# Performance work log

Hardware: AMD Instinct MI355X
Metric: run time of the kernel (lower is better)

Reference implementation:

```python
import jax, jax.numpy as jnp
import numpy as np

# Model dims (match init_kwargs)
B, H, W, C = 16, 6, 4096, 128
OVERLAP, NUM_PVQS, NUM_RVQS = 4, 3, 6
CB_DIM, CB_SIZE = 8, 1024
FIX = H * C                          # fix_dim = in_freq*in_dim = 768
HIDDEN = FIX * OVERLAP // NUM_PVQS   # 1024 per product group


def setup_inputs() -> dict:
    key = jax.random.key(0)
    k1, k2, k3, k4 = jax.random.split(key, 4)
    return {
        "z_e": jax.random.normal(k1, (B, H * W, C), jnp.float32),
        # per-(product-group, residual-stage) codebooks
        "embeds": jax.random.normal(k2, (NUM_PVQS, NUM_RVQS, CB_SIZE, CB_DIM), jnp.float32),
        # nn.Linear(hidden, codebook_dim, bias=False) stored as (hidden, cb_dim) so y = x @ W
        "proj_down": jax.random.normal(k3, (NUM_PVQS, HIDDEN, CB_DIM), jnp.float32) * (HIDDEN ** -0.5),
        "proj_up": jax.random.normal(k4, (NUM_PVQS, CB_DIM, HIDDEN), jnp.float32) * (CB_DIM ** -0.5),
        "num_streams": 6,
    }


def _l2n(x, eps=1e-12):
    return x / jnp.maximum(jnp.linalg.norm(x, axis=-1, keepdims=True), eps)


def _codebook(residual, embed):
    """One VQ codebook (l2norm variant): cdist + argmin + lookup + ST estimator.
    residual: (B, T, d); embed: (K, d)."""
    z = _l2n(residual)
    e = _l2n(embed)
    # squared euclidean distances (B, T, K)
    d = (z * z).sum(-1, keepdims=True) - 2.0 * jnp.einsum('btd,kd->btk', z, e) + (e * e).sum(-1)
    code = jnp.argmin(d, axis=-1)                      # (B, T) int
    q = jnp.take(e, code, axis=0)                      # (B, T, d)
    cb_loss = jnp.mean((q - jax.lax.stop_gradient(residual)) ** 2)
    cm_loss = jnp.mean((residual - jax.lax.stop_gradient(q)) ** 2)
    z_q = residual + jax.lax.stop_gradient(q - residual)   # straight-through
    return z_q, code, cb_loss, cm_loss


def reference(z_e, embeds, proj_down, proj_up, num_streams):
    # pre_process (dims=3): 'b (h w) c -> b w (c h)' then fold overlap frames
    x = z_e.reshape(B, H, W, C).transpose(0, 2, 3, 1).reshape(B, W, FIX)
    T = W // OVERLAP
    x = x.reshape(B, T, OVERLAP * FIX)

    zq_parts, code_parts = [], []
    cb_loss = 0.0
    cm_loss = 0.0
    for m in range(NUM_PVQS):
        xm = x[..., m * HIDDEN:(m + 1) * HIDDEN]
        residual = xm @ proj_down[m]                   # (B, T, CB_DIM)
        zq_m = jnp.zeros_like(residual)
        codes_m = []
        for i in range(num_streams):                   # residual VQ stages
            qi, ci, cb, cm = _codebook(residual, embeds[m, i])
            residual = residual - qi
            zq_m = zq_m + qi
            codes_m.append(ci)
            cb_loss = cb_loss + cb
            cm_loss = cm_loss + cm
        zq_parts.append(zq_m @ proj_up[m])             # (B, T, HIDDEN)
        code_parts.append(jnp.stack(codes_m, axis=1))  # (B, num_streams, T)

    zq = jnp.concatenate(zq_parts, axis=-1)            # (B, T, OVERLAP*FIX)
    codes = jnp.stack(code_parts, axis=2)              # (B, num_streams, num_pvqs, T)

    # post_process (dims=3): unfold overlap, 'b w (c h) -> b (h w) c'
    zq = zq.reshape(B, W, FIX).reshape(B, W, C, H).transpose(0, 3, 1, 2).reshape(B, H * W, C)
    return zq, codes, cb_loss / NUM_PVQS, cm_loss / NUM_PVQS
```

## Files before the change

kernel.cpp:

```cpp
#include <hip/hip_runtime.h>

#define BB        16
#define HH        6
#define WW        4096
#define CC        128
#define TT        1024
#define NTOK      16384
#define FIX       768
#define HID       1024
#define CBK       1024
#define CBD       8
#define NPVQ      3
#define NRVQ      6
#define ZQ_SIZE   50331648ull

#define OFF_ACC   0ull
#define OFF_EN64  16ull
#define OFF_EN32  (OFF_EN64 + 1179648ull)
#define OFF_PUT   (OFF_EN32 + 589824ull)
#define OFF_R     (OFF_PUT + 98304ull)
#define OFF_ZQ    (OFF_R + 3145728ull)

typedef float v2f __attribute__((ext_vector_type(2)));

__device__ __forceinline__ float dot32(const float* __restrict__ row,
                                       const v2f rn2[4]) {
    const float4* p4 = (const float4*)row;
    float4 e0 = p4[0], e1 = p4[1];
    v2f acc = {0.0f, 0.0f};
    v2f p;
    p.x = e0.x; p.y = e0.y; acc = __builtin_elementwise_fma(rn2[0], p, acc);
    p.x = e0.z; p.y = e0.w; acc = __builtin_elementwise_fma(rn2[1], p, acc);
    p.x = e1.x; p.y = e1.y; acc = __builtin_elementwise_fma(rn2[2], p, acc);
    p.x = e1.z; p.y = e1.w; acc = __builtin_elementwise_fma(rn2[3], p, acc);
    return acc.x + acc.y;
}

__global__ __launch_bounds__(256) void knorm(const float* __restrict__ emb,
                                             double* __restrict__ en64,
                                             float* __restrict__ en32) {
    int gid = blockIdx.x * 256 + threadIdx.x;
    if (gid >= NPVQ * NRVQ * CBK) return;
    const float* e = emb + (size_t)gid * CBD;
    double v[CBD];
    double s = 0.0;
#pragma unroll
    for (int d = 0; d < CBD; ++d) { v[d] = (double)e[d]; s += v[d] * v[d]; }
    double n = fmax(sqrt(s), 1e-12);
#pragma unroll
    for (int d = 0; d < CBD; ++d) {
        double q = v[d] / n;
        en64[(size_t)gid * CBD + d] = q;
        en32[(size_t)gid * CBD + d] = (float)q;
    }
}

__global__ __launch_bounds__(256) void kputr(const float* __restrict__ pu,
                                             float* __restrict__ pu_t) {
    int gid = blockIdx.x * 256 + threadIdx.x;
    if (gid >= NPVQ * CBD * HID) return;
    int j = gid & (HID - 1), md = gid >> 10;
    int m = md >> 3, d = md & 7;
    pu_t[((size_t)m * HID + j) * CBD + d] = pu[gid];
}

__global__ __launch_bounds__(384) void kproj(const float* __restrict__ ze,
                                             const float* __restrict__ pd,
                                             double* __restrict__ r_ws) {
    __shared__ float x[2][NPVQ * HID];
    const int tok0 = blockIdx.x * 2;
    const int b = tok0 >> 10, t0 = tok0 & 1023;
    const int tid = threadIdx.x;
    const size_t zbase = (size_t)b * (HH * WW * CC);
#pragma unroll
    for (int q = 0; q < 4; ++q) {
        int g = tid + 384 * q;
        int tk = g >= 768;
        int gg = g - tk * 768;
        int h = gg >> 7, v = gg & 127;
        const float4 val = *(const float4*)(ze + zbase + (size_t)(h * WW + (t0 + tk) * 4) * CC + v * 4);
        float vv[4] = {val.x, val.y, val.z, val.w};
#pragma unroll
        for (int e = 0; e < 4; ++e) {
            int oc = v * 4 + e, o = oc >> 7, c = oc & 127;
            x[tk][o * FIX + c * HH + h] = vv[e];
        }
    }
    __syncthreads();
    const int w = tid >> 6, l = tid & 63;
    const int tk = w >= 3, m = w - tk * 3;
    double acc[CBD] = {0, 0, 0, 0, 0, 0, 0, 0};
    for (int q = 0; q < 16; ++q) {
        int j = l + 64 * q;
        double xv = (double)x[tk][m * HID + j];
        const float* pr = pd + (size_t)(m * HID + j) * CBD;
#pragma unroll
        for (int d = 0; d < CBD; ++d) acc[d] = fma(xv, (double)pr[d], acc[d]);
    }
#pragma unroll
    for (int off = 32; off >= 1; off >>= 1) {
#pragma unroll
        for (int d = 0; d < CBD; ++d) acc[d] += __shfl_down(acc[d], off, 64);
    }
    if (l == 0) {
        double* rp = r_ws + ((size_t)m * NTOK + tok0 + tk) * CBD;
#pragma unroll
        for (int d = 0; d < CBD; ++d) rp[d] = acc[d];
    }
}

#define KV_WAVES    8
#define KV_THREADS  (KV_WAVES * 64)
#define KV_WSLICE   (CBK / KV_WAVES)
#define KV_EPS      2e-6f
#define KV_EPS_CAND 2e-6f

__global__ __launch_bounds__(KV_THREADS) void kvq(const double* __restrict__ en_all,
                                                  const float* __restrict__ es_all,
                                                  const double* __restrict__ r_ws,
                                                  float* __restrict__ zq_ws,
                                                  float* __restrict__ out,
                                                  const int* __restrict__ nsp,
                                                  double* __restrict__ accum) {
    __shared__ __align__(16) float tbl[CBK * CBD];
    __shared__ float  mb1[KV_THREADS];
    __shared__ float  mb2[KV_THREADS];
    __shared__ int    mbk[KV_THREADS];
    __shared__ double md64[KV_THREADS];
    __shared__ int    mk64[KV_THREADS];

    const int blk = blockIdx.x;
    const int m = blk >> 8, g = blk & 255;
    const int tid = threadIdx.x;
    const int w = tid >> 6, l = tid & 63;
    const int tok = g * 64 + l;
    const int b = tok >> 10, t = tok & 1023;
    const int ns = *nsp;

    double r[CBD];
    {
        const double* rp = r_ws + ((size_t)m * NTOK + tok) * CBD;
#pragma unroll
        for (int d = 0; d < CBD; ++d) r[d] = rp[d];
    }
    double zq[CBD] = {0, 0, 0, 0, 0, 0, 0, 0};
    double loss = 0.0;

    const int kl0 = w * KV_WSLICE;
    for (int i = 0; i < ns; ++i) {
        const double* en = en_all + ((size_t)(m * NRVQ + i)) * CBK * CBD;
        const float*  es = es_all + ((size_t)(m * NRVQ + i)) * CBK * CBD;
        double s = 0.0;
#pragma unroll
        for (int d = 0; d < CBD; ++d) s += r[d] * r[d];
        double inv = 1.0 / fmax(sqrt(s), 1e-12);
        v2f rn2[4];
#pragma unroll
        for (int d = 0; d < CBD; d += 2) {
            rn2[d >> 1].x = (float)(r[d] * inv);
            rn2[d >> 1].y = (float)(r[d + 1] * inv);
        }

        __syncthreads();
        {
            const float4* src = (const float4*)es;
            float4* dst = (float4*)tbl;
#pragma unroll
            for (int q = 0; q < 4; ++q) dst[tid + KV_THREADS * q] = src[tid + KV_THREADS * q];
        }
        __syncthreads();

        float b1 = -1e30f, b2 = -1e30f;
        int bk = kl0;
        for (int k = kl0; k < kl0 + KV_WSLICE; k += 4) {
            float dots[4];
#pragma unroll
            for (int u = 0; u < 4; ++u)
                dots[u] = dot32(tbl + (size_t)(k + u) * CBD, rn2);
#pragma unroll
            for (int u = 0; u < 4; ++u) {
                float dv = dots[u];
                if (dv > b1) { b2 = b1; b1 = dv; bk = k + u; }
                else if (dv > b2) { b2 = dv; }
            }
        }
        mb1[tid] = b1; mb2[tid] = b2; mbk[tid] = bk;
        __syncthreads();
        float B1 = mb1[l], B2 = mb2[l];
        int K = mbk[l];
#pragma unroll
        for (int w2 = 1; w2 < KV_WAVES; ++w2) {
            float c1 = mb1[w2 * 64 + l];
            float c2 = mb2[w2 * 64 + l];
            int   ck = mbk[w2 * 64 + l];
            if (c1 > B1) { B2 = fmaxf(B1, c2); B1 = c1; K = ck; }
            else         { B2 = fmaxf(B2, c1); }
        }
        int bbk = K;
        bool uncert = (B1 - B2) <= KV_EPS;
        if (__any(uncert)) {
            __syncthreads();
            double rb = -1e300;
            int rk = CBK;
            for (int k = kl0; k < kl0 + KV_WSLICE; ++k) {
                float dv = dot32(tbl + (size_t)k * CBD, rn2);
                if (uncert && dv >= B1 - KV_EPS_CAND) {
                    const double* e64 = en + (size_t)k * CBD;
                    double q0 = 0.0, q1 = 0.0;
#pragma unroll
                    for (int d = 0; d < CBD; d += 2) {
                        q0 = fma(r[d], e64[d], q0);
                        q1 = fma(r[d + 1], e64[d + 1], q1);
                    }
                    double dot = q0 + q1;
                    if (dot > rb || (dot == rb && k < rk)) { rb = dot; rk = k; }
                }
            }
            md64[tid] = rb; mk64[tid] = rk;
            __syncthreads();
            if (uncert) {
                double R = md64[l];
                int RK = mk64[l];
#pragma unroll
                for (int w2 = 1; w2 < KV_WAVES; ++w2) {
                    double d2 = md64[w2 * 64 + l];
                    int    k2 = mk64[w2 * 64 + l];
                    if (d2 > R || (d2 == R && k2 < RK)) { R = d2; RK = k2; }
                }
                bbk = RK;
            }
        }
        const double* qv = en + (size_t)bbk * CBD;
        if (w == 0) {
            double ls = 0.0;
#pragma unroll
            for (int d = 0; d < CBD; ++d) { double df = qv[d] - r[d]; ls += df * df; }
            loss += ls;
            out[ZQ_SIZE + ((size_t)(b * ns + i) * NPVQ + m) * TT + t] = (float)bbk;
        }
#pragma unroll
        for (int d = 0; d < CBD; ++d) { double q = qv[d]; r[d] -= q; zq[d] += q; }
    }

    if (w == 0) {
        float* zp = zq_ws + ((size_t)m * NTOK + tok) * CBD;
#pragma unroll
        for (int d = 0; d < CBD; ++d) zp[d] = (float)zq[d];
#pragma unroll
        for (int off = 32; off >= 1; off >>= 1) loss += __shfl_down(loss, off, 64);
        if (l == 0) atomicAdd(accum, loss);
    }
}

__global__ __launch_bounds__(256) void kout(const float* __restrict__ pu_t,
                                            const float* __restrict__ zq_ws,
                                            float* __restrict__ out,
                                            const int* __restrict__ nsp,
                                            const double* __restrict__ accum) {
    __shared__ float zl[32][NPVQ][CBD];
    const int blk = blockIdx.x;
    const int tok0 = blk * 32;
    const int b = tok0 >> 10, t0 = tok0 & 1023;
    const int tid = threadIdx.x;
#pragma unroll
    for (int q = 0; q < 3; ++q) {
        int ii = tid + 256 * q;
        int mm = ii >> 8, rem = ii & 255, tt = rem >> 3, d = rem & 7;
        zl[tt][mm][d] = zq_ws[((size_t)mm * NTOK + tok0 + tt) * CBD + d];
    }
    __syncthreads();
    const size_t obase = (size_t)b * (HH * WW * CC);
#pragma unroll 2
    for (int q = 0; q < 12; ++q) {
        int idx = tid + 256 * q;
        int h = idx >> 9, rem = idx & 511, o = rem >> 7, c = rem & 127;
        int f = o * FIX + c * HH + h;
        int m = f >> 10, j = f & 1023;
        const float4* p4 = (const float4*)(pu_t + ((size_t)m * HID + j) * CBD);
        float4 pa = p4[0], pb = p4[1];
        float pu8[CBD] = {pa.x, pa.y, pa.z, pa.w, pb.x, pb.y, pb.z, pb.w};
        size_t rowbase = obase + ((size_t)h * WW + t0 * 4 + o) * CC + c;
        for (int tt = 0; tt < 32; ++tt) {
            float y = 0.0f;
#pragma unroll
            for (int d = 0; d < CBD; ++d) y = fmaf(zl[tt][m][d], pu8[d], y);
            out[rowbase + (size_t)tt * 4 * CC] = y;
        }
    }
    if (blk == 0 && tid == 0) {
        int ns = *nsp;
        double s = *accum;
        float lv = (float)(s / (double)(NTOK * CBD * NPVQ));
        size_t lbase = ZQ_SIZE + (size_t)BB * ns * NPVQ * TT;
        out[lbase] = lv;
        out[lbase + 1] = lv;
    }
}

extern "C" void kernel_launch(void* const* d_in, const int* in_sizes, int n_in,
                              void* d_out, int out_size, void* d_ws, size_t ws_size,
                              hipStream_t stream) {
    const float* ze  = (const float*)d_in[0];
    const float* emb = (const float*)d_in[1];
    const float* pd  = (const float*)d_in[2];
    const float* pu  = (const float*)d_in[3];
    const int*   nsp = (const int*)d_in[4];
    float* out = (float*)d_out;
    char* ws = (char*)d_ws;

    double* accum = (double*)(ws + OFF_ACC);
    double* en64  = (double*)(ws + OFF_EN64);
    float*  en32  = (float*)(ws + OFF_EN32);
    float*  pu_t  = (float*)(ws + OFF_PUT);
    double* r_ws  = (double*)(ws + OFF_R);
    float*  zq_ws = (float*)(ws + OFF_ZQ);

    hipMemsetAsync(accum, 0, 16, stream);
    knorm<<<(NPVQ * NRVQ * CBK + 255) / 256, 256, 0, stream>>>(emb, en64, en32);
    kputr<<<(NPVQ * CBD * HID + 255) / 256, 256, 0, stream>>>(pu, pu_t);
    kproj<<<NTOK / 2, 384, 0, stream>>>(ze, pd, r_ws);
    kvq<<<NPVQ * (NTOK / 64), KV_THREADS, 0, stream>>>(en64, en32, r_ws, zq_ws, out, nsp, accum);
    kout<<<NTOK / 32, 256, 0, stream>>>(pu_t, zq_ws, out, nsp, accum);
}
```

Before: 330.0 us.

## Process four tokens per thread in VQ kernel to reuse LDS codebook loads

Each thread in the VQ search kernel now handles four tokens instead of one. Every codebook row read from LDS is reused across four token dot products, and the grid shrinks fourfold, so the per-block codebook staging into LDS is amortised over more tokens. zq accumulation moves from double to float. The costs are higher register pressure, managed with launch_bounds(512,2), fewer blocks (192) to fill the GPU, and extra syncthreads in the fallback path.

```diff
diff --git a/kernel.cpp b/kernel.cpp
--- a/kernel.cpp
+++ b/kernel.cpp
@@ -23,10 +23,8 @@
 
 typedef float v2f __attribute__((ext_vector_type(2)));
 
-__device__ __forceinline__ float dot32(const float* __restrict__ row,
-                                       const v2f rn2[4]) {
-    const float4* p4 = (const float4*)row;
-    float4 e0 = p4[0], e1 = p4[1];
+__device__ __forceinline__ float dot32v(const float4 e0, const float4 e1,
+                                        const v2f rn2[4]) {
     v2f acc = {0.0f, 0.0f};
     v2f p;
     p.x = e0.x; p.y = e0.y; acc = __builtin_elementwise_fma(rn2[0], p, acc);
@@ -111,54 +109,63 @@
 
 #define KV_WAVES    8
 #define KV_THREADS  (KV_WAVES * 64)
+#define KV_T        4
+#define KV_TPB      (64 * KV_T)
 #define KV_WSLICE   (CBK / KV_WAVES)
 #define KV_EPS      2e-6f
 #define KV_EPS_CAND 2e-6f
 
-__global__ __launch_bounds__(KV_THREADS) void kvq(const double* __restrict__ en_all,
-                                                  const float* __restrict__ es_all,
-                                                  const double* __restrict__ r_ws,
-                                                  float* __restrict__ zq_ws,
-                                                  float* __restrict__ out,
-                                                  const int* __restrict__ nsp,
-                                                  double* __restrict__ accum) {
+__global__ __launch_bounds__(KV_THREADS, 2) void kvq(const double* __restrict__ en_all,
+                                                     const float* __restrict__ es_all,
+                                                     const double* __restrict__ r_ws,
+                                                     float* __restrict__ zq_ws,
+                                                     float* __restrict__ out,
+                                                     const int* __restrict__ nsp,
+                                                     double* __restrict__ accum) {
     __shared__ __align__(16) float tbl[CBK * CBD];
-    __shared__ float  mb1[KV_THREADS];
-    __shared__ float  mb2[KV_THREADS];
-    __shared__ int    mbk[KV_THREADS];
+    __shared__ float  mb1[KV_T][KV_THREADS];
+    __shared__ float  mb2[KV_T][KV_THREADS];
+    __shared__ int    mbk[KV_T][KV_THREADS];
     __shared__ double md64[KV_THREADS];
     __shared__ int    mk64[KV_THREADS];
 
     const int blk = blockIdx.x;
-    const int m = blk >> 8, g = blk & 255;
+    const int m = blk / 64, gg = blk % 64;
     const int tid = threadIdx.x;
     const int w = tid >> 6, l = tid & 63;
-    const int tok = g * 64 + l;
-    const int b = tok >> 10, t = tok & 1023;
     const int ns = *nsp;
 
-    double r[CBD];
-    {
+    double r[KV_T][CBD];
+#pragma unroll
+    for (int j = 0; j < KV_T; ++j) {
+        const int tok = gg * KV_TPB + j * 64 + l;
         const double* rp = r_ws + ((size_t)m * NTOK + tok) * CBD;
 #pragma unroll
-        for (int d = 0; d < CBD; ++d) r[d] = rp[d];
-    }
-    double zq[CBD] = {0, 0, 0, 0, 0, 0, 0, 0};
+        for (int d = 0; d < CBD; ++d) r[j][d] = rp[d];
+    }
+    float zq[KV_T][CBD];
+#pragma unroll
+    for (int j = 0; j < KV_T; ++j)
+#pragma unroll
+        for (int d = 0; d < CBD; ++d) zq[j][d] = 0.0f;
     double loss = 0.0;
 
     const int kl0 = w * KV_WSLICE;
     for (int i = 0; i < ns; ++i) {
         const double* en = en_all + ((size_t)(m * NRVQ + i)) * CBK * CBD;
         const float*  es = es_all + ((size_t)(m * NRVQ + i)) * CBK * CBD;
-        double s = 0.0;
-#pragma unroll
-        for (int d = 0; d < CBD; ++d) s += r[d] * r[d];
-        double inv = 1.0 / fmax(sqrt(s), 1e-12);
-        v2f rn2[4];
-#pragma unroll
-        for (int d = 0; d < CBD; d += 2) {
-            rn2[d >> 1].x = (float)(r[d] * inv);
-            rn2[d >> 1].y = (float)(r[d + 1] * inv);
+        v2f rn2[KV_T][4];
+#pragma unroll
+        for (int j = 0; j < KV_T; ++j) {
+            double s = 0.0;
+#pragma unroll
+            for (int d = 0; d < CBD; ++d) s += r[j][d] * r[j][d];
+            double inv = 1.0 / fmax(sqrt(s), 1e-12);
+#pragma unroll
+            for (int d = 0; d < CBD; d += 2) {
+                rn2[j][d >> 1].x = (float)(r[j][d] * inv);
+                rn2[j][d >> 1].y = (float)(r[j][d + 1] * inv);
+            }
         }
 
         __syncthreads();
@@ -170,82 +177,119 @@
         }
         __syncthreads();
 
-        float b1 = -1e30f, b2 = -1e30f;
-        int bk = kl0;
-        for (int k = kl0; k < kl0 + KV_WSLICE; k += 4) {
-            float dots[4];
-#pragma unroll
-            for (int u = 0; u < 4; ++u)
-                dots[u] = dot32(tbl + (size_t)(k + u) * CBD, rn2);
-#pragma unroll
-            for (int u = 0; u < 4; ++u) {
-                float dv = dots[u];
-                if (dv > b1) { b2 = b1; b1 = dv; bk = k + u; }
-                else if (dv > b2) { b2 = dv; }
-            }
-        }
-        mb1[tid] = b1; mb2[tid] = b2; mbk[tid] = bk;
+        float b1[KV_T], b2[KV_T];
+        int bk[KV_T];
+#pragma unroll
+        for (int j = 0; j < KV_T; ++j) { b1[j] = -1e30f; b2[j] = -1e30f; bk[j] = kl0; }
+        for (int k = kl0; k < kl0 + KV_WSLICE; k += 2) {
+            const float4* pA = (const float4*)(tbl + (size_t)k * CBD);
+            float4 a0 = pA[0], a1 = pA[1];
+            float4 c0 = pA[2], c1 = pA[3];
+#pragma unroll
+            for (int j = 0; j < KV_T; ++j) {
+                float dA = dot32v(a0, a1, rn2[j]);
+                float dB = dot32v(c0, c1, rn2[j]);
+                if (dA > b1[j]) { b2[j] = b1[j]; b1[j] = dA; bk[j] = k; }
+                else if (dA > b2[j]) { b2[j] = dA; }
+                if (dB > b1[j]) { b2[j] = b1[j]; b1[j] = dB; bk[j] = k + 1; }
+                else if (dB > b2[j]) { b2[j] = dB; }
+            }
+        }
+#pragma unroll
+        for (int j = 0; j < KV_T; ++j) {
+            mb1[j][tid] = b1[j]; mb2[j][tid] = b2[j]; mbk[j][tid] = bk[j];
+        }
         __syncthreads();
-        float B1 = mb1[l], B2 = mb2[l];
-        int K = mbk[l];
-#pragma unroll
-        for (int w2 = 1; w2 < KV_WAVES; ++w2) {
-            float c1 = mb1[w2 * 64 + l];
-            float c2 = mb2[w2 * 64 + l];
-            int   ck = mbk[w2 * 64 + l];
-            if (c1 > B1) { B2 = fmaxf(B1, c2); B1 = c1; K = ck; }
-            else         { B2 = fmaxf(B2, c1); }
-        }
-        int bbk = K;
-        bool uncert = (B1 - B2) <= KV_EPS;
-        if (__any(uncert)) {
-            __syncthreads();
-            double rb = -1e300;
-            int rk = CBK;
+        float B1[KV_T], B2[KV_T];
+        int bbk[KV_T];
+        bool unc[KV_T];
+        bool anyu = false;
+#pragma unroll
+        for (int j = 0; j < KV_T; ++j) {
+            float x1 = mb1[j][l], x2 = mb2[j][l];
+            int xk = mbk[j][l];
+#pragma unroll
+            for (int w2 = 1; w2 < KV_WAVES; ++w2) {
+                float c1 = mb1[j][w2 * 64 + l];
+                float c2 = mb2[j][w2 * 64 + l];
+                int   ck = mbk[j][w2 * 64 + l];
+                if (c1 > x1) { x2 = fmaxf(x1, c2); x1 = c1; xk = ck; }
+                else         { x2 = fmaxf(x2, c1); }
+            }
+            B1[j] = x1; B2[j] = x2; bbk[j] = xk;
+            unc[j] = (x1 - x2) <= KV_EPS;
+            anyu |= unc[j];
+        }
+        if (__any(anyu)) {
+            double rb[KV_T];
+            int rk[KV_T];
+#pragma unroll
+            for (int j = 0; j < KV_T; ++j) { rb[j] = -1e300; rk[j] = CBK; }
             for (int k = kl0; k < kl0 + KV_WSLICE; ++k) {
-                float dv = dot32(tbl + (size_t)k * CBD, rn2);
-                if (uncert && dv >= B1 - KV_EPS_CAND) {
-                    const double* e64 = en + (size_t)k * CBD;
-                    double q0 = 0.0, q1 = 0.0;
-#pragma unroll
-                    for (int d = 0; d < CBD; d += 2) {
-                        q0 = fma(r[d], e64[d], q0);
-                        q1 = fma(r[d + 1], e64[d + 1], q1);
+                const float4* pA = (const float4*)(tbl + (size_t)k * CBD);
+                float4 e0 = pA[0], e1 = pA[1];
+#pragma unroll
+                for (int j = 0; j < KV_T; ++j) {
+                    float dv = dot32v(e0, e1, rn2[j]);
+                    if (unc[j] && dv >= B1[j] - KV_EPS_CAND) {
+                        const double* e64 = en + (size_t)k * CBD;
+                        double q0 = 0.0, q1 = 0.0;
+#pragma unroll
+                        for (int d = 0; d < CBD; d += 2) {
+                            q0 = fma(r[j][d], e64[d], q0);
+                            q1 = fma(r[j][d + 1], e64[d + 1], q1);
+                        }
+                        double dot = q0 + q1;
+                        if (dot > rb[j] || (dot == rb[j] && k < rk[j])) { rb[j] = dot; rk[j] = k; }
                     }
-                    double dot = q0 + q1;
-                    if (dot > rb || (dot == rb && k < rk)) { rb = dot; rk = k; }
                 }
             }
-            md64[tid] = rb; mk64[tid] = rk;
-            __syncthreads();
-            if (uncert) {
-                double R = md64[l];
-                int RK = mk64[l];
-#pragma unroll
-                for (int w2 = 1; w2 < KV_WAVES; ++w2) {
-                    double d2 = md64[w2 * 64 + l];
-                    int    k2 = mk64[w2 * 64 + l];
-                    if (d2 > R || (d2 == R && k2 < RK)) { R = d2; RK = k2; }
+            for (int j = 0; j < KV_T; ++j) {
+                __syncthreads();
+                md64[tid] = rb[j]; mk64[tid] = rk[j];
+                __syncthreads();
+                if (unc[j]) {
+                    double R = md64[l];
+                    int RK = mk64[l];
+#pragma unroll
+                    for (int w2 = 1; w2 < KV_WAVES; ++w2) {
+                        double d2 = md64[w2 * 64 + l];
+                        int    k2 = mk64[w2 * 64 + l];
+                        if (d2 > R || (d2 == R && k2 < RK)) { R = d2; RK = k2; }
+                    }
+                    bbk[j] = RK;
                 }
-                bbk = RK;
-            }
-        }
-        const double* qv = en + (size_t)bbk * CBD;
-        if (w == 0) {
-            double ls = 0.0;
-#pragma unroll
-            for (int d = 0; d < CBD; ++d) { double df = qv[d] - r[d]; ls += df * df; }
-            loss += ls;
-            out[ZQ_SIZE + ((size_t)(b * ns + i) * NPVQ + m) * TT + t] = (float)bbk;
-        }
-#pragma unroll
-        for (int d = 0; d < CBD; ++d) { double q = qv[d]; r[d] -= q; zq[d] += q; }
+            }
+        }
+#pragma unroll
+        for (int j = 0; j < KV_T; ++j) {
+            const double* qv = en + (size_t)bbk[j] * CBD;
+            if (w == 0) {
+                double ls = 0.0;
+#pragma unroll
+                for (int d = 0; d < CBD; ++d) { double df = qv[d] - r[j][d]; ls += df * df; }
+                loss += ls;
+                const int tok = gg * KV_TPB + j * 64 + l;
+                const int b = tok >> 10, t = tok & 1023;
+                out[ZQ_SIZE + ((size_t)(b * ns + i) * NPVQ + m) * TT + t] = (float)bbk[j];
+            }
+#pragma unroll
+            for (int d = 0; d < CBD; ++d) {
+                double q = qv[d];
+                r[j][d] -= q;
+                zq[j][d] += (float)q;
+            }
+        }
     }
 
     if (w == 0) {
-        float* zp = zq_ws + ((size_t)m * NTOK + tok) * CBD;
-#pragma unroll
-        for (int d = 0; d < CBD; ++d) zp[d] = (float)zq[d];
+#pragma unroll
+        for (int j = 0; j < KV_T; ++j) {
+            const int tok = gg * KV_TPB + j * 64 + l;
+            float* zp = zq_ws + ((size_t)m * NTOK + tok) * CBD;
+#pragma unroll
+            for (int d = 0; d < CBD; ++d) zp[d] = zq[j][d];
+        }
 #pragma unroll
         for (int off = 32; off >= 1; off >>= 1) loss += __shfl_down(loss, off, 64);
         if (l == 0) atomicAdd(accum, loss);
@@ -319,6 +363,6 @@
     knorm<<<(NPVQ * NRVQ * CBK + 255) / 256, 256, 0, stream>>>(emb, en64, en32);
     kputr<<<(NPVQ * CBD * HID + 255) / 256, 256, 0, stream>>>(pu, pu_t);
     kproj<<<NTOK / 2, 384, 0, stream>>>(ze, pd, r_ws);
-    kvq<<<NPVQ * (NTOK / 64), KV_THREADS, 0, stream>>>(en64, en32, r_ws, zq_ws, out, nsp, accum);
+    kvq<<<NPVQ * (NTOK / KV_TPB), KV_THREADS, 0, stream>>>(en64, en32, r_ws, zq_ws, out, nsp, accum);
     kout<<<NTOK / 32, 256, 0, stream>>>(pu_t, zq_ws, out, nsp, accum);
 }
```

After: 507.6 us. +53.8%, slower.

## Hold codebook in registers per lane, broadcast token vectors via LDS, single-wave VQ blocks

Applied to the files above, without the earlier changes.

The VQ kernel moves from 8-wave blocks that keep the codebook in LDS and merge per-wave top-2 results through shared memory to a single 64-thread wave. Each lane keeps 16 codebook rows in registers (32 float4) and loops over the block's 64 tokens, reading each token's normalized vector from LDS and finding the top-2 with xor-shuffle reductions. The aim is to drop LDS codebook traffic and block-wide barriers. The cost is a large register footprint, which can lower occupancy, plus about 12 shuffles per token and a serialized fp64 refinement loop for uncertain tokens. zq is now accumulated in float rather than double.

```diff
diff --git a/kernel.cpp b/kernel.cpp
--- a/kernel.cpp
+++ b/kernel.cpp
@@ -23,10 +23,8 @@
 
 typedef float v2f __attribute__((ext_vector_type(2)));
 
-__device__ __forceinline__ float dot32(const float* __restrict__ row,
-                                       const v2f rn2[4]) {
-    const float4* p4 = (const float4*)row;
-    float4 e0 = p4[0], e1 = p4[1];
+__device__ __forceinline__ float dot32v(const float4 e0, const float4 e1,
+                                        const v2f rn2[4]) {
     v2f acc = {0.0f, 0.0f};
     v2f p;
     p.x = e0.x; p.y = e0.y; acc = __builtin_elementwise_fma(rn2[0], p, acc);
@@ -109,30 +107,22 @@
     }
 }
 
-#define KV_WAVES    8
-#define KV_THREADS  (KV_WAVES * 64)
-#define KV_WSLICE   (CBK / KV_WAVES)
 #define KV_EPS      2e-6f
 #define KV_EPS_CAND 2e-6f
 
-__global__ __launch_bounds__(KV_THREADS) void kvq(const double* __restrict__ en_all,
-                                                  const float* __restrict__ es_all,
-                                                  const double* __restrict__ r_ws,
-                                                  float* __restrict__ zq_ws,
-                                                  float* __restrict__ out,
-                                                  const int* __restrict__ nsp,
-                                                  double* __restrict__ accum) {
-    __shared__ __align__(16) float tbl[CBK * CBD];
-    __shared__ float  mb1[KV_THREADS];
-    __shared__ float  mb2[KV_THREADS];
-    __shared__ int    mbk[KV_THREADS];
-    __shared__ double md64[KV_THREADS];
-    __shared__ int    mk64[KV_THREADS];
+__global__ __launch_bounds__(64) void kvq(const double* __restrict__ en_all,
+                                          const float* __restrict__ es_all,
+                                          const double* __restrict__ r_ws,
+                                          float* __restrict__ zq_ws,
+                                          float* __restrict__ out,
+                                          const int* __restrict__ nsp,
+                                          double* __restrict__ accum) {
+    __shared__ __align__(16) float  rn_sh[64][CBD];
+    __shared__ __align__(16) double rd_sh[64][CBD];
 
     const int blk = blockIdx.x;
     const int m = blk >> 8, g = blk & 255;
-    const int tid = threadIdx.x;
-    const int w = tid >> 6, l = tid & 63;
+    const int l = threadIdx.x;
     const int tok = g * 64 + l;
     const int b = tok >> 10, t = tok & 1023;
     const int ns = *nsp;
@@ -143,113 +133,150 @@
 #pragma unroll
         for (int d = 0; d < CBD; ++d) r[d] = rp[d];
     }
-    double zq[CBD] = {0, 0, 0, 0, 0, 0, 0, 0};
+    float zq[CBD];
+#pragma unroll
+    for (int d = 0; d < CBD; ++d) zq[d] = 0.0f;
     double loss = 0.0;
 
-    const int kl0 = w * KV_WSLICE;
     for (int i = 0; i < ns; ++i) {
         const double* en = en_all + ((size_t)(m * NRVQ + i)) * CBK * CBD;
         const float*  es = es_all + ((size_t)(m * NRVQ + i)) * CBK * CBD;
+
         double s = 0.0;
 #pragma unroll
         for (int d = 0; d < CBD; ++d) s += r[d] * r[d];
         double inv = 1.0 / fmax(sqrt(s), 1e-12);
-        v2f rn2[4];
-#pragma unroll
-        for (int d = 0; d < CBD; d += 2) {
-            rn2[d >> 1].x = (float)(r[d] * inv);
-            rn2[d >> 1].y = (float)(r[d + 1] * inv);
-        }
+        float rn[CBD];
+#pragma unroll
+        for (int d = 0; d < CBD; ++d) rn[d] = (float)(r[d] * inv);
 
         __syncthreads();
+        *(float4*)&rn_sh[l][0] = make_float4(rn[0], rn[1], rn[2], rn[3]);
+        *(float4*)&rn_sh[l][4] = make_float4(rn[4], rn[5], rn[6], rn[7]);
+
+        float4 cb[32];
         {
             const float4* src = (const float4*)es;
-            float4* dst = (float4*)tbl;
-#pragma unroll
-            for (int q = 0; q < 4; ++q) dst[tid + KV_THREADS * q] = src[tid + KV_THREADS * q];
+#pragma unroll
+            for (int c = 0; c < 16; ++c) {
+                cb[2 * c]     = src[c * 128 + l * 2];
+                cb[2 * c + 1] = src[c * 128 + l * 2 + 1];
+            }
         }
         __syncthreads();
 
-        float b1 = -1e30f, b2 = -1e30f;
-        int bk = kl0;
-        for (int k = kl0; k < kl0 + KV_WSLICE; k += 4) {
-            float dots[4];
-#pragma unroll
-            for (int u = 0; u < 4; ++u)
-                dots[u] = dot32(tbl + (size_t)(k + u) * CBD, rn2);
-#pragma unroll
-            for (int u = 0; u < 4; ++u) {
-                float dv = dots[u];
-                if (dv > b1) { b2 = b1; b1 = dv; bk = k + u; }
+        float myB1 = 0.0f;
+        int   myK  = 0;
+        bool  myUnc = false;
+
+#pragma unroll 2
+        for (int j = 0; j < 64; ++j) {
+            float4 ra = *(const float4*)&rn_sh[j][0];
+            float4 rb4 = *(const float4*)&rn_sh[j][4];
+            v2f rB[4];
+            rB[0].x = ra.x;  rB[0].y = ra.y;
+            rB[1].x = ra.z;  rB[1].y = ra.w;
+            rB[2].x = rb4.x; rB[2].y = rb4.y;
+            rB[3].x = rb4.z; rB[3].y = rb4.w;
+
+            float b1 = -1e30f, b2 = -1e30f;
+            int bk = l;
+#pragma unroll
+            for (int c = 0; c < 16; ++c) {
+                float dv = dot32v(cb[2 * c], cb[2 * c + 1], rB);
+                if (dv > b1) { b2 = b1; b1 = dv; bk = c * 64 + l; }
                 else if (dv > b2) { b2 = dv; }
             }
-        }
-        mb1[tid] = b1; mb2[tid] = b2; mbk[tid] = bk;
-        __syncthreads();
-        float B1 = mb1[l], B2 = mb2[l];
-        int K = mbk[l];
-#pragma unroll
-        for (int w2 = 1; w2 < KV_WAVES; ++w2) {
-            float c1 = mb1[w2 * 64 + l];
-            float c2 = mb2[w2 * 64 + l];
-            int   ck = mbk[w2 * 64 + l];
-            if (c1 > B1) { B2 = fmaxf(B1, c2); B1 = c1; K = ck; }
-            else         { B2 = fmaxf(B2, c1); }
-        }
-        int bbk = K;
-        bool uncert = (B1 - B2) <= KV_EPS;
-        if (__any(uncert)) {
+            float g1 = b1, g2 = b2;
+#pragma unroll
+            for (int mask = 1; mask < 64; mask <<= 1) {
+                float o1 = __shfl_xor(g1, mask, 64);
+                float o2 = __shfl_xor(g2, mask, 64);
+                float hi = fmaxf(g1, o1);
+                float lo = fminf(g1, o1);
+                g2 = fmaxf(fmaxf(g2, o2), lo);
+                g1 = hi;
+            }
+            unsigned long long mk = __ballot(b1 == g1);
+            int src = __ffsll(mk) - 1;
+            int K = __shfl(bk, src, 64);
+            bool uj = (g1 - g2) <= KV_EPS;
+            if (l == j) { myB1 = g1; myK = K; myUnc = uj; }
+        }
+
+        unsigned long long um = __ballot(myUnc);
+        if (um) {
+            *(double2*)&rd_sh[l][0] = make_double2(r[0], r[1]);
+            *(double2*)&rd_sh[l][2] = make_double2(r[2], r[3]);
+            *(double2*)&rd_sh[l][4] = make_double2(r[4], r[5]);
+            *(double2*)&rd_sh[l][6] = make_double2(r[6], r[7]);
             __syncthreads();
-            double rb = -1e300;
-            int rk = CBK;
-            for (int k = kl0; k < kl0 + KV_WSLICE; ++k) {
-                float dv = dot32(tbl + (size_t)k * CBD, rn2);
-                if (uncert && dv >= B1 - KV_EPS_CAND) {
-                    const double* e64 = en + (size_t)k * CBD;
-                    double q0 = 0.0, q1 = 0.0;
-#pragma unroll
-                    for (int d = 0; d < CBD; d += 2) {
-                        q0 = fma(r[d], e64[d], q0);
-                        q1 = fma(r[d + 1], e64[d + 1], q1);
+            while (um) {
+                int j = __ffsll(um) - 1;
+                um &= um - 1;
+                float B1j = __shfl(myB1, j, 64);
+                float4 ra = *(const float4*)&rn_sh[j][0];
+                float4 rb4 = *(const float4*)&rn_sh[j][4];
+                v2f rB[4];
+                rB[0].x = ra.x;  rB[0].y = ra.y;
+                rB[1].x = ra.z;  rB[1].y = ra.w;
+                rB[2].x = rb4.x; rB[2].y = rb4.y;
+                rB[3].x = rb4.z; rB[3].y = rb4.w;
+                double rj[CBD];
+#pragma unroll
+                for (int d = 0; d < CBD; ++d) rj[d] = rd_sh[j][d];
+                double rb = -1e300;
+                int rk = CBK;
+#pragma unroll
+                for (int c = 0; c < 16; ++c) {
+                    float dv = dot32v(cb[2 * c], cb[2 * c + 1], rB);
+                    int kk = c * 64 + l;
+                    if (dv >= B1j - KV_EPS_CAND) {
+                        const double* e64 = en + (size_t)kk * CBD;
+                        double q0 = 0.0, q1 = 0.0;
+#pragma unroll
+                        for (int d = 0; d < CBD; d += 2) {
+                            q0 = fma(rj[d], e64[d], q0);
+                            q1 = fma(rj[d + 1], e64[d + 1], q1);
+                        }
+                        double dot = q0 + q1;
+                        if (dot > rb || (dot == rb && kk < rk)) { rb = dot; rk = kk; }
                     }
-                    double dot = q0 + q1;
-                    if (dot > rb || (dot == rb && k < rk)) { rb = dot; rk = k; }
                 }
+#pragma unroll
+                for (int mask = 1; mask < 64; mask <<= 1) {
+                    double ov = __shfl_xor(rb, mask, 64);
+                    int    ok = __shfl_xor(rk, mask, 64);
+                    bool take = (ov > rb) || (ov == rb && ok < rk);
+                    rb = take ? ov : rb;
+                    rk = take ? ok : rk;
+                }
+                if (l == j) myK = rk;
             }
-            md64[tid] = rb; mk64[tid] = rk;
-            __syncthreads();
-            if (uncert) {
-                double R = md64[l];
-                int RK = mk64[l];
-#pragma unroll
-                for (int w2 = 1; w2 < KV_WAVES; ++w2) {
-                    double d2 = md64[w2 * 64 + l];
-                    int    k2 = mk64[w2 * 64 + l];
-                    if (d2 > R || (d2 == R && k2 < RK)) { R = d2; RK = k2; }
-                }
-                bbk = RK;
-            }
-        }
-        const double* qv = en + (size_t)bbk * CBD;
-        if (w == 0) {
-            double ls = 0.0;
-#pragma unroll
-            for (int d = 0; d < CBD; ++d) { double df = qv[d] - r[d]; ls += df * df; }
-            loss += ls;
-            out[ZQ_SIZE + ((size_t)(b * ns + i) * NPVQ + m) * TT + t] = (float)bbk;
-        }
-#pragma unroll
-        for (int d = 0; d < CBD; ++d) { double q = qv[d]; r[d] -= q; zq[d] += q; }
-    }
-
-    if (w == 0) {
+        }
+
+        const double* qv = en + (size_t)myK * CBD;
+        double ls = 0.0;
+#pragma unroll
+        for (int d = 0; d < CBD; ++d) {
+            double q = qv[d];
+            double df = q - r[d];
+            ls += df * df;
+            r[d] -= q;
+            zq[d] += (float)q;
+        }
+        loss += ls;
+        out[ZQ_SIZE + ((size_t)(b * ns + i) * NPVQ + m) * TT + t] = (float)myK;
+    }
+
+    {
         float* zp = zq_ws + ((size_t)m * NTOK + tok) * CBD;
-#pragma unroll
-        for (int d = 0; d < CBD; ++d) zp[d] = (float)zq[d];
-#pragma unroll
-        for (int off = 32; off >= 1; off >>= 1) loss += __shfl_down(loss, off, 64);
-        if (l == 0) atomicAdd(accum, loss);
-    }
+        *(float4*)&zp[0] = make_float4(zq[0], zq[1], zq[2], zq[3]);
+        *(float4*)&zp[4] = make_float4(zq[4], zq[5], zq[6], zq[7]);
+    }
+#pragma unroll
+    for (int off = 32; off >= 1; off >>= 1) loss += __shfl_down(loss, off, 64);
+    if (l == 0) atomicAdd(accum, loss);
 }
 
 __global__ __launch_bounds__(256) void kout(const float* __restrict__ pu_t,
@@ -319,6 +346,6 @@
     knorm<<<(NPVQ * NRVQ * CBK + 255) / 256, 256, 0, stream>>>(emb, en64, en32);
     kputr<<<(NPVQ * CBD * HID + 255) / 256, 256, 0, stream>>>(pu, pu_t);
     kproj<<<NTOK / 2, 384, 0, stream>>>(ze, pd, r_ws);
-    kvq<<<NPVQ * (NTOK / 64), KV_THREADS, 0, stream>>>(en64, en32, r_ws, zq_ws, out, nsp, accum);
+    kvq<<<NPVQ * (NTOK / 64), 64, 0, stream>>>(en64, en32, r_ws, zq_ws, out, nsp, accum);
     kout<<<NTOK / 32, 256, 0, stream>>>(pu_t, zq_ws, out, nsp, accum);
 }
```

Result: slower. 565.6 us (+71.4%).

## Read codebook directly from global memory via VGPR pointer instead of LDS staging

Applied to the files above, without the earlier changes.

Removes the per-stage copy of the float codebook into shared memory and the two barriers around it. Instead each thread loads codebook rows from global memory with float4 loads, using an inline-asm VGPR pointer to keep them as vector memory loads. It also adds a minimum-blocks occupancy hint and accumulates zq in float instead of double. This trades LDS broadcast reads for cached global loads, and risks higher load latency in the inner distance loop.

```diff
diff --git a/kernel.cpp b/kernel.cpp
--- a/kernel.cpp
+++ b/kernel.cpp
@@ -23,10 +23,8 @@
 
 typedef float v2f __attribute__((ext_vector_type(2)));
 
-__device__ __forceinline__ float dot32(const float* __restrict__ row,
-                                       const v2f rn2[4]) {
-    const float4* p4 = (const float4*)row;
-    float4 e0 = p4[0], e1 = p4[1];
+__device__ __forceinline__ float dot32v(const float4 e0, const float4 e1,
+                                        const v2f rn2[4]) {
     v2f acc = {0.0f, 0.0f};
     v2f p;
     p.x = e0.x; p.y = e0.y; acc = __builtin_elementwise_fma(rn2[0], p, acc);
@@ -34,6 +32,16 @@
     p.x = e1.x; p.y = e1.y; acc = __builtin_elementwise_fma(rn2[2], p, acc);
     p.x = e1.z; p.y = e1.w; acc = __builtin_elementwise_fma(rn2[3], p, acc);
     return acc.x + acc.y;
+}
+
+__device__ __forceinline__ const float* opaque_vgpr(const float* p) {
+    uint64_t u = (uint64_t)(uintptr_t)p;
+    uint32_t lo = (uint32_t)u, hi = (uint32_t)(u >> 32);
+    uint32_t vlo, vhi;
+    asm volatile("v_mov_b32 %0, %2\n\tv_mov_b32 %1, %3"
+                 : "=v"(vlo), "=v"(vhi)
+                 : "s"(lo), "s"(hi));
+    return (const float*)(((uint64_t)vhi << 32) | (uint64_t)vlo);
 }
 
 __global__ __launch_bounds__(256) void knorm(const float* __restrict__ emb,
@@ -115,14 +123,13 @@
 #define KV_EPS      2e-6f
 #define KV_EPS_CAND 2e-6f
 
-__global__ __launch_bounds__(KV_THREADS) void kvq(const double* __restrict__ en_all,
-                                                  const float* __restrict__ es_all,
-                                                  const double* __restrict__ r_ws,
-                                                  float* __restrict__ zq_ws,
-                                                  float* __restrict__ out,
-                                                  const int* __restrict__ nsp,
-                                                  double* __restrict__ accum) {
-    __shared__ __align__(16) float tbl[CBK * CBD];
+__global__ __launch_bounds__(KV_THREADS, 2) void kvq(const double* __restrict__ en_all,
+                                                     const float* __restrict__ es_all,
+                                                     const double* __restrict__ r_ws,
+                                                     float* __restrict__ zq_ws,
+                                                     float* __restrict__ out,
+                                                     const int* __restrict__ nsp,
+                                                     double* __restrict__ accum) {
     __shared__ float  mb1[KV_THREADS];
     __shared__ float  mb2[KV_THREADS];
     __shared__ int    mbk[KV_THREADS];
@@ -137,19 +144,23 @@
     const int b = tok >> 10, t = tok & 1023;
     const int ns = *nsp;
 
+    const float* esv = opaque_vgpr(es_all);
+
     double r[CBD];
     {
         const double* rp = r_ws + ((size_t)m * NTOK + tok) * CBD;
 #pragma unroll
         for (int d = 0; d < CBD; ++d) r[d] = rp[d];
     }
-    double zq[CBD] = {0, 0, 0, 0, 0, 0, 0, 0};
+    float zq[CBD];
+#pragma unroll
+    for (int d = 0; d < CBD; ++d) zq[d] = 0.0f;
     double loss = 0.0;
 
     const int kl0 = w * KV_WSLICE;
     for (int i = 0; i < ns; ++i) {
-        const double* en = en_all + ((size_t)(m * NRVQ + i)) * CBK * CBD;
-        const float*  es = es_all + ((size_t)(m * NRVQ + i)) * CBK * CBD;
+        const double* en  = en_all + ((size_t)(m * NRVQ + i)) * CBK * CBD;
+        const float*  esi = esv    + ((size_t)(m * NRVQ + i)) * CBK * CBD;
         double s = 0.0;
 #pragma unroll
         for (int d = 0; d < CBD; ++d) s += r[d] * r[d];
@@ -161,22 +172,19 @@
             rn2[d >> 1].y = (float)(r[d + 1] * inv);
         }
 
-        __syncthreads();
-        {
-            const float4* src = (const float4*)es;
-            float4* dst = (float4*)tbl;
-#pragma unroll
-            for (int q = 0; q < 4; ++q) dst[tid + KV_THREADS * q] = src[tid + KV_THREADS * q];
-        }
-        __syncthreads();
-
         float b1 = -1e30f, b2 = -1e30f;
         int bk = kl0;
         for (int k = kl0; k < kl0 + KV_WSLICE; k += 4) {
+            const float4* pA = (const float4*)esi + (size_t)k * 2;
+            float4 e0 = pA[0], e1 = pA[1];
+            float4 e2 = pA[2], e3 = pA[3];
+            float4 e4 = pA[4], e5 = pA[5];
+            float4 e6 = pA[6], e7 = pA[7];
             float dots[4];
-#pragma unroll
-            for (int u = 0; u < 4; ++u)
-                dots[u] = dot32(tbl + (size_t)(k + u) * CBD, rn2);
+            dots[0] = dot32v(e0, e1, rn2);
+            dots[1] = dot32v(e2, e3, rn2);
+            dots[2] = dot32v(e4, e5, rn2);
+            dots[3] = dot32v(e6, e7, rn2);
 #pragma unroll
             for (int u = 0; u < 4; ++u) {
                 float dv = dots[u];
@@ -184,6 +192,7 @@
                 else if (dv > b2) { b2 = dv; }
             }
         }
+        __syncthreads();
         mb1[tid] = b1; mb2[tid] = b2; mbk[tid] = bk;
         __syncthreads();
         float B1 = mb1[l], B2 = mb2[l];
@@ -203,7 +212,8 @@
             double rb = -1e300;
             int rk = CBK;
             for (int k = kl0; k < kl0 + KV_WSLICE; ++k) {
-                float dv = dot32(tbl + (size_t)k * CBD, rn2);
+                const float4* pA = (const float4*)esi + (size_t)k * 2;
+                float dv = dot32v(pA[0], pA[1], rn2);
                 if (uncert && dv >= B1 - KV_EPS_CAND) {
                     const double* e64 = en + (size_t)k * CBD;
                     double q0 = 0.0, q1 = 0.0;
@@ -239,13 +249,17 @@
             out[ZQ_SIZE + ((size_t)(b * ns + i) * NPVQ + m) * TT + t] = (float)bbk;
         }
 #pragma unroll
-        for (int d = 0; d < CBD; ++d) { double q = qv[d]; r[d] -= q; zq[d] += q; }
+        for (int d = 0; d < CBD; ++d) {
+            double q = qv[d];
+            r[d] -= q;
+            zq[d] += (float)q;
+        }
     }
 
     if (w == 0) {
         float* zp = zq_ws + ((size_t)m * NTOK + tok) * CBD;
 #pragma unroll
-        for (int d = 0; d < CBD; ++d) zp[d] = (float)zq[d];
+        for (int d = 0; d < CBD; ++d) zp[d] = zq[d];
 #pragma unroll
         for (int off = 32; off >= 1; off >>= 1) loss += __shfl_down(loss, off, 64);
         if (l == 0) atomicAdd(accum, loss);
```

New measurement: 489.3 us. +48.3%, slower.
